# Performance work log

Measured on AMD Instinct MI355X. Metric: run time of the kernel, lower is better.

## Reference

```python
import jax, jax.numpy as jnp
import numpy as np

N, E, B = 50000, 800000, 1000
NODE_DIN, BB_DOUT, DHID, K = 32, 64, 64, 3
GLOB_DIN, EMBED_DIN = 64, 64
CIN = BB_DOUT + NODE_DIN  # 96


def setup_inputs() -> dict:
    key = jax.random.key(0)
    ks = jax.random.split(key, 24)

    def w(k, shape, fan_in):
        return jax.random.normal(k, shape, jnp.float32) / np.float32(np.sqrt(fan_in))

    inp = dict(
        x=jax.random.normal(ks[0], (N, NODE_DIN), jnp.float32),
        u=jax.random.normal(ks[1], (B, GLOB_DIN), jnp.float32),
        z=jax.random.normal(ks[2], (N, BB_DOUT), jnp.float32),
        edge_index=jax.random.randint(ks[3], (2, E), 0, N),
        edge_weight=jax.random.uniform(ks[4], (E,), jnp.float32),
        batch=jnp.sort(jax.random.randint(ks[5], (N,), 0, B)),
        batch_size=B,
        prev_h=jax.random.normal(ks[6], (N, DHID), jnp.float32),
    )
    # six ChebConvs of GConvGRU: x-convs take CIN, h-convs take DHID; all output DHID
    for i, nm in enumerate(["xz", "hz", "xr", "hr", "xh", "hh"]):
        cin = CIN if nm[0] == "x" else DHID
        inp[f"W{nm}"] = w(ks[7 + 2 * i], (K, cin, DHID), cin * K)
        inp[f"b{nm}"] = jnp.zeros((DHID,), jnp.float32)
    inp["Wg"] = w(ks[20], (GLOB_DIN, EMBED_DIN), GLOB_DIN)
    inp["bg"] = jnp.zeros((EMBED_DIN,), jnp.float32)
    return inp


def _cheb(xin, W, b, src, dst, w_norm, n):
    """ChebConv with sym norm, lambda_max=2 -> L_hat = -D^-1/2 A D^-1/2 (diag cancels)."""
    def prop(t):  # L_hat @ t  ([N,C])
        return -jax.ops.segment_sum(w_norm[:, None] * t[src], dst, num_segments=n)

    out = xin @ W[0] + b
    tx_prev = xin
    tx = None
    if W.shape[0] > 1:
        tx = prop(xin)
        out = out + tx @ W[1]
    for k in range(2, W.shape[0]):
        tx_new = 2.0 * prop(tx) - tx_prev
        out = out + tx_new @ W[k]
        tx_prev, tx = tx, tx_new
    return out


def reference(x, u, z, edge_index, edge_weight, batch, batch_size, prev_h,
              Wxz, bxz, Whz, bhz, Wxr, bxr, Whr, bhr, Wxh, bxh, Whh, bhh, Wg, bg):
    n = x.shape[0]
    src, dst = edge_index[0], edge_index[1]
    deg = jax.ops.segment_sum(edge_weight, src, num_segments=n)
    deg_safe = jnp.where(deg > 0, deg, 1.0)
    dinv = jnp.where(deg > 0, jax.lax.rsqrt(deg_safe), 0.0)
    w_norm = dinv[src] * edge_weight * dinv[dst]

    xin = jnp.concatenate([z, x], axis=-1)  # [N, CIN]
    Z = jax.nn.sigmoid(_cheb(xin, Wxz, bxz, src, dst, w_norm, n)
                       + _cheb(prev_h, Whz, bhz, src, dst, w_norm, n))
    R = jax.nn.sigmoid(_cheb(xin, Wxr, bxr, src, dst, w_norm, n)
                       + _cheb(prev_h, Whr, bhr, src, dst, w_norm, n))
    Ht = jnp.tanh(_cheb(xin, Wxh, bxh, src, dst, w_norm, n)
                  + _cheb(prev_h * R, Whh, bhh, src, dst, w_norm, n))
    h = Z * prev_h + (1.0 - Z) * Ht

    graph_emb = jax.ops.segment_sum(z, batch, num_segments=batch_size)  # [B, BB_DOUT]
    global_emb = jax.nn.relu(u @ Wg + bg)                                # [B, EMBED_DIN]
    fused = jnp.concatenate([graph_emb, global_emb], axis=-1)           # [B, 128]
    return fused, h
```

## Files before the change

kernel.cpp:

```cpp
#include <hip/hip_runtime.h>

#define NN 50000
#define EE 800000
#define BB 1000
#define NB 196
#define NR 8
#define RS 6272
#define NC 32
#define CHUNK 25000

typedef unsigned short u16;
typedef __attribute__((ext_vector_type(8))) short bf16x8;
typedef __attribute__((ext_vector_type(4))) float f32x4;

static __device__ __forceinline__ u16 f2b(float f) {
    union { float f; unsigned u; } v;
    v.f = f;
    unsigned r = v.u + 0x7fffu + ((v.u >> 16) & 1u);
    return (u16)(r >> 16);
}

static __device__ __forceinline__ float b2f(short s) {
    union { unsigned u; float f; } c;
    c.u = ((unsigned)(u16)s) << 16;
    return c.f;
}

__global__ __launch_bounds__(512) void k_degcnt_lds(
    const int* __restrict__ src, const int* __restrict__ dst,
    const float* __restrict__ ew, float* __restrict__ deg_p,
    int* __restrict__ cnt_p) {
    __shared__ float sdeg[RS];
    __shared__ int scnt[RS];
    int r = blockIdx.x & (NR - 1);
    int c = blockIdx.x >> 3;
    int base = r * RS;
    for (int i = threadIdx.x; i < RS; i += 512) {
        sdeg[i] = 0.f;
        scnt[i] = 0;
    }
    __syncthreads();
    int e0 = c * CHUNK;
    for (int j = threadIdx.x; j < CHUNK; j += 512) {
        int e = e0 + j;
        int s = src[e], d = dst[e];
        int sl = s - base, dl = d - base;
        if ((unsigned)sl < RS) atomicAdd(&sdeg[sl], ew[e]);
        if ((unsigned)dl < RS) atomicAdd(&scnt[dl], 1);
    }
    __syncthreads();
    int lim = (NN - base < RS) ? (NN - base) : RS;
    for (int i = threadIdx.x; i < lim; i += 512) {
        deg_p[(size_t)c * NN + base + i] = sdeg[i];
        cnt_p[(size_t)c * NN + base + i] = scnt[i];
    }
}

__global__ void k_scan1(const int* __restrict__ cnt_p, int* __restrict__ cnt,
                        int* __restrict__ incl, int* __restrict__ bsum) {
    __shared__ int s[256];
    int i = blockIdx.x * 256 + threadIdx.x;
    int v = 0;
    if (i < NN) {
#pragma unroll
        for (int p = 0; p < NC; p++) v += cnt_p[(size_t)p * NN + i];
        cnt[i] = v;
    }
    s[threadIdx.x] = v;
    __syncthreads();
    for (int off = 1; off < 256; off <<= 1) {
        int t = (threadIdx.x >= off) ? s[threadIdx.x - off] : 0;
        __syncthreads();
        s[threadIdx.x] += t;
        __syncthreads();
    }
    if (i < NN) incl[i] = s[threadIdx.x];
    if (threadIdx.x == 255) bsum[blockIdx.x] = s[255];
}

__global__ void k_scan2(int* __restrict__ bsum) {
    __shared__ int s[256];
    int v = (threadIdx.x < NB) ? bsum[threadIdx.x] : 0;
    s[threadIdx.x] = v;
    __syncthreads();
    for (int off = 1; off < 256; off <<= 1) {
        int t = (threadIdx.x >= off) ? s[threadIdx.x - off] : 0;
        __syncthreads();
        s[threadIdx.x] += t;
        __syncthreads();
    }
    if (threadIdx.x < NB) bsum[threadIdx.x] = s[threadIdx.x];
}

__global__ void k_scan3(const int* __restrict__ incl, const int* __restrict__ cnt,
                        const int* __restrict__ bsum, int* __restrict__ row_ptr,
                        int* __restrict__ cursor, const float* __restrict__ deg_p,
                        float* __restrict__ dinv) {
    int i = blockIdx.x * 256 + threadIdx.x;
    if (i >= NN) return;
    int off = (blockIdx.x > 0) ? bsum[blockIdx.x - 1] : 0;
    int start = off + incl[i] - cnt[i];
    row_ptr[i] = start;
    cursor[i] = start;
    float d = 0.f;
#pragma unroll
    for (int p = 0; p < NC; p++) d += deg_p[(size_t)p * NN + i];
    dinv[i] = d > 0.f ? rsqrtf(d) : 0.f;
}

__global__ void k_scatter(const int* __restrict__ src, const int* __restrict__ dst,
                          const float* __restrict__ ew, const float* __restrict__ dinv,
                          int* __restrict__ cursor, uint2* __restrict__ csr8) {
    int e = blockIdx.x * 256 + threadIdx.x;
    if (e >= EE) return;
    int d = dst[e], s = src[e];
    int pos = atomicAdd(&cursor[d], 1);
    float w = dinv[s] * ew[e] * dinv[d];
    csr8[pos] = make_uint2((unsigned)s, __float_as_uint(w));
}

__global__ void k_build_A(const float* __restrict__ z, const float* __restrict__ x,
                          const float* __restrict__ ph, u16* __restrict__ A) {
    int i = blockIdx.x * 256 + threadIdx.x;
    if (i >= NN * 160) return;
    int n = i / 160, c = i - n * 160;
    float v;
    if (c < 64) v = z[n * 64 + c];
    else if (c < 96) v = x[n * 32 + (c - 64)];
    else v = ph[n * 64 + (c - 96)];
    A[(size_t)n * 480 + c] = f2b(v);
}

__global__ void k_packW_all(const float* __restrict__ Wxz, const float* __restrict__ Wxr,
                            const float* __restrict__ Wxh, const float* __restrict__ Whz,
                            const float* __restrict__ Whr, const float* __restrict__ Whh,
                            u16* __restrict__ Wp, u16* __restrict__ W3p) {
    int idx = blockIdx.x * 256 + threadIdx.x;
    if (idx < 15 * 12 * 512) {
        int j = idx & 7, l = (idx >> 3) & 63;
        int ct = (idx >> 9) % 12, s = (idx >> 9) / 12;
        int k = 32 * s + (l >> 4) * 8 + j;
        int g = ct >> 2;
        int c = 16 * (ct & 3) + (l & 15);
        bool isX;
        int kr;
        if (k < 96)       { isX = true;  kr = k; }
        else if (k < 160) { isX = false; kr = k - 96; }
        else if (k < 256) { isX = true;  kr = 96 + (k - 160); }
        else if (k < 320) { isX = false; kr = 64 + (k - 256); }
        else if (k < 416) { isX = true;  kr = 192 + (k - 320); }
        else              { isX = false; kr = 128 + (k - 416); }
        float val;
        if (isX) {
            const float* W = (g == 0) ? Wxz : ((g == 1) ? Wxr : Wxh);
            val = W[kr * 64 + c];
        } else if (g == 2) {
            val = 0.f;
        } else {
            const float* W = (g == 0) ? Whz : Whr;
            val = W[kr * 64 + c];
        }
        Wp[idx] = f2b(val);
    } else {
        int i2 = idx - 15 * 12 * 512;
        if (i2 >= 6 * 4 * 512) return;
        int j = i2 & 7, l = (i2 >> 3) & 63;
        int ct = (i2 >> 9) & 3, s = i2 >> 11;
        int k = 32 * s + (l >> 4) * 8 + j;
        int ki = k >> 6, kr = k & 63;
        int c = 16 * ct + (l & 15);
        W3p[i2] = f2b(Whh[(ki * 64 + kr) * 64 + c]);
    }
}

template <int C, int SCALE, bool HB, int BS, int OS>
__global__ __launch_bounds__(BS) void k_pull(
    const u16* __restrict__ Abase, int inofs, int baseofs, int outofs,
    const uint2* __restrict__ csr8, const int* __restrict__ row_ptr,
    const int* __restrict__ cnt) {
    constexpr int TPR = C / 8;
    int tid = blockIdx.x * BS + threadIdx.x;
    int r = tid / TPR;
    int c8 = (tid - r * TPR) * 8;
    if (r >= NN) return;
    int s0 = row_ptr[r], n = cnt[r];
    float acc[8] = {0.f, 0.f, 0.f, 0.f, 0.f, 0.f, 0.f, 0.f};
    const u16* in = Abase + inofs + c8;
    uint2 e = (n > 0) ? csr8[s0] : make_uint2(0u, 0u);
    for (int j = 0; j < n; j++) {
        uint2 ec = e;
        if (j + 1 < n) e = csr8[s0 + j + 1];
        float w = __uint_as_float(ec.y);
        bf16x8 v = *(const bf16x8*)(in + (size_t)ec.x * OS);
#pragma unroll
        for (int k = 0; k < 8; k++) acc[k] += w * b2f(v[k]);
    }
    const float sc = -(float)SCALE;
    float o[8];
    if (HB) {
        bf16x8 b = *(const bf16x8*)(Abase + (size_t)r * OS + baseofs + c8);
#pragma unroll
        for (int k = 0; k < 8; k++) o[k] = sc * acc[k] - b2f(b[k]);
    } else {
#pragma unroll
        for (int k = 0; k < 8; k++) o[k] = sc * acc[k];
    }
    bf16x8 p;
#pragma unroll
    for (int k = 0; k < 8; k++) p[k] = (short)f2b(o[k]);
    *(bf16x8*)(const_cast<u16*>(Abase) + (size_t)r * OS + outofs + c8) = p;
}

__global__ __launch_bounds__(256) void k_gates_mfma(
    const u16* __restrict__ A, const u16* __restrict__ Wp,
    const float* __restrict__ bxz, const float* __restrict__ bhz,
    const float* __restrict__ bxr, const float* __restrict__ bhr,
    const float* __restrict__ bxh,
    u16* __restrict__ Zb16, u16* __restrict__ Hx16, u16* __restrict__ A3) {
    int wv = (blockIdx.x * 256 + threadIdx.x) >> 6;
    int lane = threadIdx.x & 63;
    int r0 = wv * 16;
    if (r0 >= NN) return;
    int q = lane >> 4, j0 = lane & 15;

    f32x4 acc[12];
#pragma unroll
    for (int i = 0; i < 12; i++) acc[i] = (f32x4){0.f, 0.f, 0.f, 0.f};

    const u16* arow = A + (size_t)(r0 + j0) * 480 + q * 8;
#pragma unroll
    for (int s = 0; s < 15; s++) {
        bf16x8 a = *(const bf16x8*)(arow + 32 * s);
        const u16* bp = Wp + (size_t)(s * 12) * 512 + lane * 8;
#pragma unroll
        for (int ct = 0; ct < 12; ct++) {
            bf16x8 b = *(const bf16x8*)(bp + ct * 512);
            acc[ct] = __builtin_amdgcn_mfma_f32_16x16x32_bf16(a, b, acc[ct], 0, 0, 0);
        }
    }

#pragma unroll
    for (int ct = 0; ct < 4; ct++) {
        int j = 16 * ct + j0;
        float bz = bxz[j] + bhz[j];
        float br = bxr[j] + bhr[j];
        float bh = bxh[j];
#pragma unroll
        for (int reg = 0; reg < 4; reg++) {
            int r = r0 + q * 4 + reg;
            size_t i = (size_t)r * 64 + j;
            float zp = acc[ct][reg] + bz;
            float rp = acc[ct + 4][reg] + br;
            float hp = acc[ct + 8][reg] + bh;
            float zv = 1.f / (1.f + expf(-zp));
            float rv = 1.f / (1.f + expf(-rp));
            float phv = b2f((short)A[(size_t)r * 480 + 96 + j]);
            Zb16[i] = f2b(zv);
            Hx16[i] = f2b(hp);
            A3[(size_t)r * 192 + j] = f2b(rv * phv);
        }
    }
}

__global__ __launch_bounds__(256) void k_final_mfma(
    const u16* __restrict__ A3, const u16* __restrict__ W3p,
    const float* __restrict__ bhh, const u16* __restrict__ Hx16,
    const u16* __restrict__ Zb16, const u16* __restrict__ A,
    float* __restrict__ outh) {
    int wv = (blockIdx.x * 256 + threadIdx.x) >> 6;
    int lane = threadIdx.x & 63;
    int r0 = wv * 16;
    if (r0 >= NN) return;
    int q = lane >> 4, j0 = lane & 15;

    f32x4 acc[4];
#pragma unroll
    for (int i = 0; i < 4; i++) acc[i] = (f32x4){0.f, 0.f, 0.f, 0.f};

    const u16* arow = A3 + (size_t)(r0 + j0) * 192 + q * 8;
#pragma unroll
    for (int s = 0; s < 6; s++) {
        bf16x8 a = *(const bf16x8*)(arow + 32 * s);
        const u16* bp = W3p + (size_t)(s * 4) * 512 + lane * 8;
#pragma unroll
        for (int ct = 0; ct < 4; ct++) {
            bf16x8 b = *(const bf16x8*)(bp + ct * 512);
            acc[ct] = __builtin_amdgcn_mfma_f32_16x16x32_bf16(a, b, acc[ct], 0, 0, 0);
        }
    }

#pragma unroll
    for (int ct = 0; ct < 4; ct++) {
        int j = 16 * ct + j0;
        float bh = bhh[j];
#pragma unroll
        for (int reg = 0; reg < 4; reg++) {
            int r = r0 + q * 4 + reg;
            size_t i = (size_t)r * 64 + j;
            float ht = tanhf(b2f((short)Hx16[i]) + acc[ct][reg] + bh);
            float zv = b2f((short)Zb16[i]);
            float phv = b2f((short)A[(size_t)r * 480 + 96 + j]);
            outh[i] = zv * phv + (1.f - zv) * ht;
        }
    }
}

__global__ __launch_bounds__(256) void k_tail(
    const float* __restrict__ z, const int* __restrict__ batch,
    const float* __restrict__ u, const float* __restrict__ Wg,
    const float* __restrict__ bg, float* __restrict__ out) {
    int b = (blockIdx.x * 256 + threadIdx.x) >> 6;
    int lane = threadIdx.x & 63;
    if (b >= BB) return;
    int lo = 0, hi = NN;
    while (lo < hi) {
        int m = (lo + hi) >> 1;
        if (batch[m] < b) lo = m + 1; else hi = m;
    }
    int start = lo;
    hi = NN;
    while (lo < hi) {
        int m = (lo + hi) >> 1;
        if (batch[m] < b + 1) lo = m + 1; else hi = m;
    }
    int end = lo;
    float acc = 0.f;
    for (int n = start; n < end; n++) acc += z[(size_t)n * 64 + lane];
    float g = bg[lane];
    const float* ur = u + (size_t)b * 64;
    for (int k = 0; k < 64; k++) g += ur[k] * Wg[k * 64 + lane];
    g = fmaxf(g, 0.f);
    out[(size_t)b * 128 + lane] = acc;
    out[(size_t)b * 128 + 64 + lane] = g;
}

extern "C" void kernel_launch(void* const* d_in, const int* in_sizes, int n_in,
                              void* d_out, int out_size, void* d_ws, size_t ws_size,
                              hipStream_t stream) {
    const float* x  = (const float*)d_in[0];
    const float* u  = (const float*)d_in[1];
    const float* z  = (const float*)d_in[2];
    const int*   ei = (const int*)d_in[3];
    const float* ew = (const float*)d_in[4];
    const int* batch = (const int*)d_in[5];
    const float* ph = (const float*)d_in[7];
    const float *Wxz = (const float*)d_in[8],  *bxz = (const float*)d_in[9];
    const float *Whz = (const float*)d_in[10], *bhz = (const float*)d_in[11];
    const float *Wxr = (const float*)d_in[12], *bxr = (const float*)d_in[13];
    const float *Whr = (const float*)d_in[14], *bhr = (const float*)d_in[15];
    const float *Wxh = (const float*)d_in[16], *bxh = (const float*)d_in[17];
    const float *Whh = (const float*)d_in[18], *bhh = (const float*)d_in[19];
    const float *Wg  = (const float*)d_in[20], *bg  = (const float*)d_in[21];
    const int* src = ei;
    const int* dst = ei + EE;

    char* wsb = (char*)d_ws;
    size_t o = 0;
    auto alloc = [&](size_t bytes) {
        void* p = wsb + o;
        o += (bytes + 255) & ~(size_t)255;
        return p;
    };
    float* deg_p   = (float*)alloc((size_t)NC * NN * 4);
    int*   cnt_p   = (int*)alloc((size_t)NC * NN * 4);
    int*   cnt     = (int*)alloc(NN * 4);
    int*   incl    = (int*)alloc(NN * 4);
    int*   row_ptr = (int*)alloc(NN * 4);
    int*   cursor  = (int*)alloc(NN * 4);
    float* dinv    = (float*)alloc(NN * 4);
    int*   bsum    = (int*)alloc(256 * 4);
    uint2* csr8    = (uint2*)alloc((size_t)EE * 8);
    u16*   Zb16 = (u16*)alloc((size_t)NN * 64 * 2);
    u16*   Hx16 = (u16*)alloc((size_t)NN * 64 * 2);
    u16*   A    = (u16*)alloc((size_t)NN * 480 * 2);
    u16*   A3   = (u16*)alloc((size_t)NN * 192 * 2);
    u16*   Wp   = (u16*)alloc(15 * 12 * 512 * 2);
    u16*   W3p  = (u16*)alloc(6 * 4 * 512 * 2);

    float* outF = (float*)d_out;
    float* outH = outF + (size_t)BB * 128;

    const int BLK = 256;
    const int gE = (EE + BLK - 1) / BLK;
    const int gA = (NN * 160 + BLK - 1) / BLK;
    const int gPull160 = (NN + 15) / 16;
    const int gPull64 = (NN + 31) / 32;
    const int gMFMA = (3125 + 3) / 4;
    const int gPack = (15 * 12 * 512 + 6 * 4 * 512 + BLK - 1) / BLK;

    k_packW_all<<<gPack, BLK, 0, stream>>>(Wxz, Wxr, Wxh, Whz, Whr, Whh, Wp, W3p);
    k_build_A<<<gA, BLK, 0, stream>>>(z, x, ph, A);

    k_degcnt_lds<<<NR * NC, 512, 0, stream>>>(src, dst, ew, deg_p, cnt_p);

    k_scan1<<<NB, 256, 0, stream>>>(cnt_p, cnt, incl, bsum);
    k_scan2<<<1, 256, 0, stream>>>(bsum);
    k_scan3<<<NB, 256, 0, stream>>>(incl, cnt, bsum, row_ptr, cursor, deg_p, dinv);
    k_scatter<<<gE, BLK, 0, stream>>>(src, dst, ew, dinv, cursor, csr8);

    k_pull<160, 1, false, 320, 480><<<gPull160, 320, 0, stream>>>(A, 0, 0, 160, csr8, row_ptr, cnt);
    k_pull<160, 2, true, 320, 480><<<gPull160, 320, 0, stream>>>(A, 160, 0, 320, csr8, row_ptr, cnt);

    k_gates_mfma<<<gMFMA, BLK, 0, stream>>>(A, Wp, bxz, bhz, bxr, bhr, bxh, Zb16, Hx16, A3);

    k_pull<64, 1, false, 256, 192><<<gPull64, 256, 0, stream>>>(A3, 0, 0, 64, csr8, row_ptr, cnt);
    k_pull<64, 2, true, 256, 192><<<gPull64, 256, 0, stream>>>(A3, 64, 0, 128, csr8, row_ptr, cnt);

    k_final_mfma<<<gMFMA, BLK, 0, stream>>>(A3, W3p, bhh, Hx16, Zb16, A, outH);

    k_tail<<<(BB * 64 + BLK - 1) / BLK, BLK, 0, stream>>>(z, batch, u, Wg, bg, outF);
}
```

Baseline: 432.3 us.

## Build CSR via two-pass bucket sort instead of global atomic scatter

The per-edge global atomicAdd scatter into CSR is replaced by two kernels. The first bins edges into 160 destination row-ranges, using LDS counters and one global atomic per bin per block, and writes packed 64-bit records into a staging buffer that reuses the deg_p workspace. The second sorts each row-range's records into LDS and writes the CSR slice back out coalesced. This is meant to remove scattered, contended global atomics and random 8-byte writes, at the cost of an extra pass over the edges and a packing that requires node ids below 65536.

Measured after the change: 407.6 us (median of 2 runs). 1.06x faster.

```diff
diff --git a/kernel.cpp b/kernel.cpp
--- a/kernel.cpp
+++ b/kernel.cpp
@@ -9,7 +9,14 @@
 #define NC 32
 #define CHUNK 25000
 
+#define NRB 160
+#define RSB 314
+#define NBIN 256
+#define CH2 3125
+#define CAP 7000
+
 typedef unsigned short u16;
+typedef unsigned long long u64;
 typedef __attribute__((ext_vector_type(8))) short bf16x8;
 typedef __attribute__((ext_vector_type(4))) float f32x4;
 
@@ -94,29 +101,71 @@
 
 __global__ void k_scan3(const int* __restrict__ incl, const int* __restrict__ cnt,
                         const int* __restrict__ bsum, int* __restrict__ row_ptr,
-                        int* __restrict__ cursor, const float* __restrict__ deg_p,
+                        int* __restrict__ scur, const float* __restrict__ deg_p,
                         float* __restrict__ dinv) {
     int i = blockIdx.x * 256 + threadIdx.x;
     if (i >= NN) return;
     int off = (blockIdx.x > 0) ? bsum[blockIdx.x - 1] : 0;
     int start = off + incl[i] - cnt[i];
     row_ptr[i] = start;
-    cursor[i] = start;
+    if (i % RSB == 0) scur[i / RSB] = start;
     float d = 0.f;
 #pragma unroll
     for (int p = 0; p < NC; p++) d += deg_p[(size_t)p * NN + i];
     dinv[i] = d > 0.f ? rsqrtf(d) : 0.f;
 }
 
-__global__ void k_scatter(const int* __restrict__ src, const int* __restrict__ dst,
-                          const float* __restrict__ ew, const float* __restrict__ dinv,
-                          int* __restrict__ cursor, uint2* __restrict__ csr8) {
-    int e = blockIdx.x * 256 + threadIdx.x;
-    if (e >= EE) return;
-    int d = dst[e], s = src[e];
-    int pos = atomicAdd(&cursor[d], 1);
-    float w = dinv[s] * ew[e] * dinv[d];
-    csr8[pos] = make_uint2((unsigned)s, __float_as_uint(w));
+__global__ __launch_bounds__(512) void k_bin(
+    const int* __restrict__ src, const int* __restrict__ dst,
+    const float* __restrict__ ew, const float* __restrict__ dinv,
+    int* __restrict__ scur, u64* __restrict__ stage) {
+    __shared__ int cntA[NRB], baseB[NRB], rk[NRB];
+    int e0 = blockIdx.x * CH2;
+    for (int i = threadIdx.x; i < NRB; i += 512) cntA[i] = 0;
+    __syncthreads();
+    for (int j = threadIdx.x; j < CH2; j += 512) {
+        int d = dst[e0 + j];
+        atomicAdd(&cntA[d / RSB], 1);
+    }
+    __syncthreads();
+    for (int i = threadIdx.x; i < NRB; i += 512) {
+        baseB[i] = atomicAdd(&scur[i], cntA[i]);
+        rk[i] = 0;
+    }
+    __syncthreads();
+    for (int j = threadIdx.x; j < CH2; j += 512) {
+        int e = e0 + j;
+        int d = dst[e], s = src[e];
+        int r = d / RSB;
+        int slot = baseB[r] + atomicAdd(&rk[r], 1);
+        float w = dinv[s] * ew[e] * dinv[d];
+        unsigned dl = (unsigned)(d - r * RSB);
+        u64 rec = ((u64)((dl << 16) | (unsigned)s) << 32) | (u64)__float_as_uint(w);
+        stage[slot] = rec;
+    }
+}
+
+__global__ __launch_bounds__(512) void k_sortrange(
+    const u64* __restrict__ stage, const int* __restrict__ row_ptr,
+    uint2* __restrict__ csr8) {
+    __shared__ uint2 img[CAP];
+    __shared__ int cur[RSB];
+    int r = blockIdx.x;
+    int r0 = r * RSB;
+    int nrows = (NN - r0 < RSB) ? (NN - r0) : RSB;
+    int p0 = row_ptr[r0];
+    int p1 = (r0 + nrows < NN) ? row_ptr[r0 + nrows] : EE;
+    for (int i = threadIdx.x; i < nrows; i += 512) cur[i] = row_ptr[r0 + i] - p0;
+    __syncthreads();
+    int n = p1 - p0;
+    for (int j = threadIdx.x; j < n; j += 512) {
+        u64 rec = stage[p0 + j];
+        unsigned hi = (unsigned)(rec >> 32);
+        int pos = atomicAdd(&cur[hi >> 16], 1);
+        img[pos] = make_uint2(hi & 0xffffu, (unsigned)(rec & 0xffffffffu));
+    }
+    __syncthreads();
+    for (int j = threadIdx.x; j < n; j += 512) csr8[p0 + j] = img[j];
 }
 
 __global__ void k_build_A(const float* __restrict__ z, const float* __restrict__ x,
@@ -366,9 +415,9 @@
     int*   cnt     = (int*)alloc(NN * 4);
     int*   incl    = (int*)alloc(NN * 4);
     int*   row_ptr = (int*)alloc(NN * 4);
-    int*   cursor  = (int*)alloc(NN * 4);
     float* dinv    = (float*)alloc(NN * 4);
     int*   bsum    = (int*)alloc(256 * 4);
+    int*   scur    = (int*)alloc(NRB * 4);
     uint2* csr8    = (uint2*)alloc((size_t)EE * 8);
     u16*   Zb16 = (u16*)alloc((size_t)NN * 64 * 2);
     u16*   Hx16 = (u16*)alloc((size_t)NN * 64 * 2);
@@ -376,12 +425,12 @@
     u16*   A3   = (u16*)alloc((size_t)NN * 192 * 2);
     u16*   Wp   = (u16*)alloc(15 * 12 * 512 * 2);
     u16*   W3p  = (u16*)alloc(6 * 4 * 512 * 2);
+    u64*   stage = (u64*)deg_p;
 
     float* outF = (float*)d_out;
     float* outH = outF + (size_t)BB * 128;
 
     const int BLK = 256;
-    const int gE = (EE + BLK - 1) / BLK;
     const int gA = (NN * 160 + BLK - 1) / BLK;
     const int gPull160 = (NN + 15) / 16;
     const int gPull64 = (NN + 31) / 32;
@@ -395,8 +444,10 @@
 
     k_scan1<<<NB, 256, 0, stream>>>(cnt_p, cnt, incl, bsum);
     k_scan2<<<1, 256, 0, stream>>>(bsum);
-    k_scan3<<<NB, 256, 0, stream>>>(incl, cnt, bsum, row_ptr, cursor, deg_p, dinv);
-    k_scatter<<<gE, BLK, 0, stream>>>(src, dst, ew, dinv, cursor, csr8);
+    k_scan3<<<NB, 256, 0, stream>>>(incl, cnt, bsum, row_ptr, scur, deg_p, dinv);
+
+    k_bin<<<NBIN, 512, 0, stream>>>(src, dst, ew, dinv, scur, stage);
+    k_sortrange<<<NRB, 512, 0, stream>>>(stage, row_ptr, csr8);
 
     k_pull<160, 1, false, 320, 480><<<gPull160, 320, 0, stream>>>(A, 0, 0, 160, csr8, row_ptr, cnt);
     k_pull<160, 2, true, 320, 480><<<gPull160, 320, 0, stream>>>(A, 160, 0, 320, csr8, row_ptr, cnt);
```
